# Kernel tuning notes

Measured on AMD Instinct MI355X. Metric: run time of the kernel, lower is better.

## Reference

```python
import jax, jax.numpy as jnp
import numpy as np

N_HEAD = 16
N_EMBD = 2048
B, S = 2, 2048


def setup_inputs() -> dict:
    key = jax.random.key(0)
    k1, k2, k3 = jax.random.split(key, 3)
    scale = 0.02
    return {
        "hidden_states": jax.random.normal(k1, (B, S, N_EMBD), dtype=jnp.float32),
        "attention_mask": jnp.ones((B, S), dtype=jnp.float32),
        "w_attn": jax.random.normal(k2, (N_EMBD, 3 * N_EMBD), dtype=jnp.float32) * scale,
        "b_attn": jnp.zeros((3 * N_EMBD,), dtype=jnp.float32),
        "w_proj": jax.random.normal(k3, (N_EMBD, N_EMBD), dtype=jnp.float32) * scale,
        "b_proj": jnp.zeros((N_EMBD,), dtype=jnp.float32),
    }


def reference(hidden_states, attention_mask, w_attn, b_attn, w_proj, b_proj):
    b, s, d = hidden_states.shape
    h = N_HEAD
    dh = d // h
    qkv = hidden_states @ w_attn + b_attn          # [b, s, 3d]
    q, k, v = jnp.split(qkv, 3, axis=-1)
    # [b, s, d] -> [b, h, s, dh]
    q = q.reshape(b, s, h, dh).transpose(0, 2, 1, 3)
    k = k.reshape(b, s, h, dh).transpose(0, 2, 1, 3)
    v = v.reshape(b, s, h, dh).transpose(0, 2, 1, 3)
    scores = jnp.einsum("bhqd,bhkd->bhqk", q, k) / jnp.sqrt(jnp.float32(dh))
    # padding mask: [b, s] -> additive bias [b, 1, 1, s]
    bias = (1.0 - attention_mask)[:, None, None, :] * -10000.0
    attn = jax.nn.softmax(scores + bias, axis=-1)   # dropout p=0 (eval)
    out = jnp.einsum("bhqk,bhkd->bhqd", attn, v)    # [b, h, s, dh]
    out = out.transpose(0, 2, 1, 3).reshape(b, s, d)
    return out @ w_proj + b_proj
```

## Files before the change

kernel.cpp:

```cpp
#include <hip/hip_runtime.h>
#include <stdint.h>

#define B_   2
#define S_   2048
#define D_   2048
#define NH_  16
#define DH_  128
#define N3_  6144

typedef unsigned short u16;
typedef __bf16 bf16x8 __attribute__((ext_vector_type(8)));
typedef float  f32x4  __attribute__((ext_vector_type(4)));

#define QSCALE   (0.08838834764831845f * 1.4426950408889634f)
#define BIASF    (-10000.0f * 1.4426950408889634f)

__device__ __forceinline__ u16 f2bf(float f) {
  union { float f; unsigned u; } v; v.f = f;
  unsigned u = v.u;
  return (u16)((u + 0x7FFFu + ((u >> 16) & 1u)) >> 16);
}

__device__ __forceinline__ float fast_exp2(float x) {
  float r;
  asm("v_exp_f32 %0, %1" : "=v"(r) : "v"(x));
  return r;
}

#define GL2LDS(gsrc, ldst)                                                              \
  __builtin_amdgcn_global_load_lds((const __attribute__((address_space(1))) void*)(gsrc), \
      (__attribute__((address_space(3))) void*)(ldst), 16, 0, 0)

__device__ __forceinline__ int swz_id() {
  int id = blockIdx.y * gridDim.x + blockIdx.x;
  int cpx = (gridDim.x * gridDim.y) >> 3;
  return (id & 7) * cpx + (id >> 3);
}

__global__ void cvt_kernel(const float* __restrict__ in, u16* __restrict__ out, int n4) {
  int i = blockIdx.x * blockDim.x + threadIdx.x;
  int stride = gridDim.x * blockDim.x;
  for (; i < n4; i += stride) {
    float4 v = ((const float4*)in)[i];
    ushort4 o;
    o.x = f2bf(v.x); o.y = f2bf(v.y); o.z = f2bf(v.z); o.w = f2bf(v.w);
    ((ushort4*)out)[i] = o;
  }
}

__global__ void transpose_kernel(const float* __restrict__ in, u16* __restrict__ out,
                                 int K, int N) {
  __shared__ float tile[32][33];
  int tx = threadIdx.x, ty = threadIdx.y;
  int nx = blockIdx.x * 32, ky = blockIdx.y * 32;
#pragma unroll
  for (int j = 0; j < 32; j += 8)
    tile[ty + j][tx] = in[(size_t)(ky + ty + j) * N + nx + tx];
  __syncthreads();
#pragma unroll
  for (int j = 0; j < 32; j += 8)
    out[(size_t)(nx + ty + j) * K + ky + tx] = f2bf(tile[tx][ty + j]);
}


__device__ __forceinline__ void read_q(const u16* __restrict__ Ab, const u16* __restrict__ Bb,
                                       int wrB, int wcB, int g, int lr,
                                       bf16x8 (&AF)[4][2], bf16x8 (&BF)[2][2]) {
#pragma unroll
  for (int i = 0; i < 4; ++i) {
    int hr = wrB + i * 16 + lr;
#pragma unroll
    for (int kk = 0; kk < 2; ++kk)
      AF[i][kk] = *reinterpret_cast<const bf16x8*>(Ab + hr * 64 + ((((kk << 2) | g) ^ (hr & 7)) * 8));
  }
#pragma unroll
  for (int j = 0; j < 2; ++j) {
    int hbr = wcB + j * 16 + lr;
#pragma unroll
    for (int kk = 0; kk < 2; ++kk)
      BF[j][kk] = *reinterpret_cast<const bf16x8*>(Bb + hbr * 64 + ((((kk << 2) | g) ^ (hbr & 7)) * 8));
  }
}

template <int MS, int NS>
__device__ __forceinline__ void mfma_q(const bf16x8 (&AF)[4][2], const bf16x8 (&BF)[2][2],
                                       f32x4 (&acc)[8][4]) {
  __builtin_amdgcn_s_setprio(1);
#pragma unroll
  for (int i = 0; i < 4; ++i)
#pragma unroll
    for (int j = 0; j < 2; ++j)
#pragma unroll
      for (int kk = 0; kk < 2; ++kk)
        acc[MS * 4 + i][NS * 2 + j] = __builtin_amdgcn_mfma_f32_16x16x32_bf16(
            AF[i][kk], BF[j][kk], acc[MS * 4 + i][NS * 2 + j], 0, 0, 0);
  __builtin_amdgcn_s_setprio(0);
}

template <int KD>
__device__ __forceinline__ void stage_a(const u16* __restrict__ A, u16* lds,
                                        int c, int h, int Tg, int m0, int t) {
#pragma unroll
  for (int inst = 0; inst < 2; ++inst) {
    int idx = inst * 512 + t, hr = idx >> 3, slot = idx & 7;
    int trow = ((hr >> 6) << 7) + h * 64 + (hr & 63);
    GL2LDS(A + (size_t)(m0 + trow) * KD + Tg * 64 + ((slot ^ (hr & 7)) * 8),
           lds + c * 32768 + h * 8192 + idx * 8);
  }
}

template <int KD>
__device__ __forceinline__ void stage_b(const u16* __restrict__ BT, u16* lds,
                                        int c, int h, int Tg, int n0, int t) {
#pragma unroll
  for (int inst = 0; inst < 2; ++inst) {
    int idx = inst * 512 + t, hr = idx >> 3, slot = idx & 7;
    int n = ((hr >> 5) << 6) + h * 32 + (hr & 31);
    GL2LDS(BT + (size_t)(n0 + n) * KD + Tg * 64 + ((slot ^ (hr & 7)) * 8),
           lds + c * 32768 + 16384 + h * 8192 + idx * 8);
  }
}

#define ABASE(c, h) (lds + (c) * 32768 + (h) * 8192)
#define BBASE(c, h) (lds + (c) * 32768 + 16384 + (h) * 8192)
#define VMCNT(n) asm volatile("s_waitcnt vmcnt(" #n ")" ::: "memory")
#define LGKM0                                            \
  do {                                                   \
    asm volatile("s_waitcnt lgkmcnt(0)" ::: "memory");   \
    __builtin_amdgcn_sched_barrier(0);                   \
  } while (0)
#define BAR __builtin_amdgcn_s_barrier()

template <int KD>
__device__ __forceinline__ void gemm256_core(const u16* __restrict__ A, const u16* __restrict__ BT,
                                             int m0, int n0, u16* lds, f32x4 (&acc)[8][4]) {
  const int NT = KD / 64;
  int t = threadIdx.x, wv = t >> 6, lane = t & 63;
  int g = lane >> 4, lr = lane & 15;
  int wrB = (wv >> 2) * 64, wcB = (wv & 3) * 32;
  bf16x8 af0[4][2], bf0[2][2], af1[4][2], bf1[2][2];

  stage_b<KD>(BT, lds, 0, 0, 0, n0, t);
  stage_a<KD>(A, lds, 0, 0, 0, m0, t);
  stage_a<KD>(A, lds, 0, 1, 0, m0, t);
  stage_b<KD>(BT, lds, 0, 1, 0, n0, t);
  stage_b<KD>(BT, lds, 1, 0, 1, n0, t);
  stage_a<KD>(A, lds, 1, 0, 1, m0, t);
  VMCNT(2);
  stage_a<KD>(A, lds, 1, 1, 1, m0, t);
  stage_b<KD>(BT, lds, 1, 1, 1, n0, t);
  BAR;
  read_q(ABASE(0, 0), BBASE(0, 0), wrB, wcB, g, lr, af0, bf0);
  LGKM0;

  for (int T = 0; T < NT; ++T) {
    int c = T & 1;
    read_q(ABASE(c, 1), BBASE(c, 0), wrB, wcB, g, lr, af1, bf1);
    BAR; LGKM0;
    mfma_q<0, 0>(af0, bf0, acc);
    BAR;
    read_q(ABASE(c, 0), BBASE(c, 1), wrB, wcB, g, lr, af0, bf0);
    if (T + 2 < NT) stage_b<KD>(BT, lds, c, 0, T + 2, n0, t);
    BAR; LGKM0;
    mfma_q<1, 0>(af1, bf1, acc);
    BAR;
    read_q(ABASE(c, 1), BBASE(c, 1), wrB, wcB, g, lr, af1, bf1);
    if (T + 2 < NT) stage_a<KD>(A, lds, c, 0, T + 2, m0, t);
    BAR; LGKM0;
    mfma_q<0, 1>(af0, bf0, acc);
    BAR;
    if (T + 2 < NT) {
      VMCNT(2);
      stage_a<KD>(A, lds, c, 1, T + 2, m0, t);
      stage_b<KD>(BT, lds, c, 1, T + 2, n0, t);
    } else {
      VMCNT(0);
    }
    BAR;
    if (T + 1 < NT) read_q(ABASE(c ^ 1, 0), BBASE(c ^ 1, 0), wrB, wcB, g, lr, af0, bf0);
    LGKM0;
    mfma_q<1, 1>(af1, bf1, acc);
    BAR;
  }
}

__global__ __launch_bounds__(512, 1) void gemm_qkv_kernel(
    const u16* __restrict__ A, const u16* __restrict__ BT, const float* __restrict__ bias,
    u16* __restrict__ Qb, u16* __restrict__ Kb, u16* __restrict__ VTb) {
  __shared__ __attribute__((aligned(16))) u16 lds[65536];
  f32x4 acc[8][4] = {};
  int sw = swz_id();
  int n0 = (sw % gridDim.x) * 256, m0 = (sw / gridDim.x) * 256;
  gemm256_core<2048>(A, BT, m0, n0, lds, acc);
  int t = threadIdx.x, lane = t & 63, wv = t >> 6;
  int g = lane >> 4, lr = lane & 15, wr = wv >> 2, wc = wv & 3;
#pragma unroll
  for (int mi = 0; mi < 8; ++mi) {
    int rowbase = m0 + wr * 128 + mi * 16 + g * 4;
    int b = rowbase >> 11, s = rowbase & 2047;
#pragma unroll
    for (int nj = 0; nj < 4; ++nj) {
      int col = n0 + wc * 64 + nj * 16 + lr;
      float bv = bias[col];
      int sec = col >> 11;
      int within = col & 2047;
      int h = within >> 7, d = within & 127;
      if (sec < 2) {
        float mult = (sec == 0) ? QSCALE : 1.0f;
        u16* dst = (sec == 0 ? Qb : Kb) + ((size_t)(b * NH_ + h) * S_ + s) * DH_ + d;
#pragma unroll
        for (int r = 0; r < 4; ++r) dst[(size_t)r * DH_] = f2bf((acc[mi][nj][r] + bv) * mult);
      } else {
        u16* dst = VTb + ((size_t)(b * NH_ + h) * DH_ + d) * S_ + s;
        ushort4 pk;
        pk.x = f2bf(acc[mi][nj][0] + bv); pk.y = f2bf(acc[mi][nj][1] + bv);
        pk.z = f2bf(acc[mi][nj][2] + bv); pk.w = f2bf(acc[mi][nj][3] + bv);
        *reinterpret_cast<ushort4*>(dst) = pk;
      }
    }
  }
}

__global__ __launch_bounds__(512, 1) void gemm_proj_kernel(
    const u16* __restrict__ A, const u16* __restrict__ BT, const float* __restrict__ bias,
    float* __restrict__ out) {
  __shared__ __attribute__((aligned(16))) u16 lds[65536];
  f32x4 acc[8][4] = {};
  int sw = swz_id();
  int n0 = (sw % gridDim.x) * 256, m0 = (sw / gridDim.x) * 256;
  gemm256_core<2048>(A, BT, m0, n0, lds, acc);
  int t = threadIdx.x, lane = t & 63, wv = t >> 6;
  int g = lane >> 4, lr = lane & 15, wr = wv >> 2, wc = wv & 3;
#pragma unroll
  for (int mi = 0; mi < 8; ++mi) {
    int rowbase = m0 + wr * 128 + mi * 16 + g * 4;
#pragma unroll
    for (int nj = 0; nj < 4; ++nj) {
      int col = n0 + wc * 64 + nj * 16 + lr;
      float bv = bias[col];
      float* dst = out + (size_t)rowbase * D_ + col;
#pragma unroll
      for (int r = 0; r < 4; ++r) dst[(size_t)r * D_] = acc[mi][nj][r] + bv;
    }
  }
}

__global__ __launch_bounds__(256) void attn_kernel(
    const u16* __restrict__ Qb, const u16* __restrict__ Kb, const u16* __restrict__ VTb,
    const float* __restrict__ mask, u16* __restrict__ AO) {
  __shared__ __attribute__((aligned(16))) u16 Ks[2][64 * 128];
  __shared__ __attribute__((aligned(16))) u16 Vs[2][128 * 64];
  __shared__ __attribute__((aligned(16))) u16 Ps[4][16 * 64];
  __shared__ float bias_lds[S_];

  int t = threadIdx.x, w = t >> 6, lane = t & 63;
  int g = lane >> 4, lr = lane & 15;
  int sw = swz_id();
  int qt = sw & 31, bh = sw >> 5;
  int b = bh >> 4;
  const u16* Qh = Qb + (size_t)bh * S_ * DH_;
  const u16* Kh = Kb + (size_t)bh * S_ * DH_;
  const u16* Vh = VTb + (size_t)bh * DH_ * S_;
  int q0 = qt * 64 + w * 16;

  for (int i = t; i < S_; i += 256)
    bias_lds[i] = (1.0f - mask[b * S_ + i]) * BIASF;

  bf16x8 aq[4];
#pragma unroll
  for (int kk = 0; kk < 4; ++kk)
    aq[kk] = *reinterpret_cast<const bf16x8*>(Qh + (size_t)(q0 + lr) * DH_ + kk * 32 + g * 8);

  f32x4 oacc[8] = {};
  float m_r[4], l_r[4];
#pragma unroll
  for (int r = 0; r < 4; ++r) { m_r[r] = -1e30f; l_r[r] = 0.f; }

  __syncthreads();

#define STAGE_KV(buf, s0base)                                                    \
  {                                                                              \
    _Pragma("unroll")                                                            \
    for (int i = 0; i < 4; ++i) {                                                \
      int idx = i * 256 + t;                                                     \
      int row = idx >> 4, slot = idx & 15;                                       \
      GL2LDS(Kh + (size_t)((s0base) + row) * DH_ + ((slot ^ (row & 7)) * 8),     \
             &Ks[buf][idx * 8]);                                                 \
    }                                                                            \
    _Pragma("unroll")                                                            \
    for (int i = 0; i < 4; ++i) {                                                \
      int idx = i * 256 + t;                                                     \
      int row = idx >> 3, slot = idx & 7;                                        \
      GL2LDS(Vh + (size_t)row * S_ + (s0base) + ((slot ^ (row & 7)) * 8),        \
             &Vs[buf][idx * 8]);                                                 \
    }                                                                            \
  }

  STAGE_KV(0, 0);
  const int NT = S_ / 64;
  for (int it = 0; it < NT; ++it) {
    int cur = it & 1;
    if (it + 1 < NT) {
      STAGE_KV(cur ^ 1, (it + 1) * 64);
      asm volatile("s_waitcnt vmcnt(8)" ::: "memory");
    } else {
      asm volatile("s_waitcnt vmcnt(0)" ::: "memory");
    }
    __builtin_amdgcn_s_barrier();
    __builtin_amdgcn_sched_barrier(0);

    f32x4 sacc[4] = {};
#pragma unroll
    for (int kk = 0; kk < 4; ++kk) {
#pragma unroll
      for (int n = 0; n < 4; ++n) {
        int c = lr + 16 * n;
        bf16x8 bk = *reinterpret_cast<const bf16x8*>(
            &Ks[cur][c * 128 + ((((kk << 2) | g) ^ (c & 7)) * 8)]);
        sacc[n] = __builtin_amdgcn_mfma_f32_16x16x32_bf16(aq[kk], bk, sacc[n], 0, 0, 0);
      }
    }

    int s0 = it * 64;
    float sv[4][4], mx[4];
#pragma unroll
    for (int r = 0; r < 4; ++r) {
#pragma unroll
      for (int n = 0; n < 4; ++n) sv[r][n] = sacc[n][r] + bias_lds[s0 + lr + 16 * n];
      float m2 = fmaxf(fmaxf(sv[r][0], sv[r][1]), fmaxf(sv[r][2], sv[r][3]));
#pragma unroll
      for (int off = 1; off < 16; off <<= 1) m2 = fmaxf(m2, __shfl_xor(m2, off));
      mx[r] = m2;
    }
    float gmax = fmaxf(fmaxf(mx[0] - m_r[0], mx[1] - m_r[1]),
                       fmaxf(mx[2] - m_r[2], mx[3] - m_r[3]));
    if (__any(gmax > 8.f)) {
#pragma unroll
      for (int r = 0; r < 4; ++r) {
        float mnew = fmaxf(m_r[r], mx[r]);
        float f = fast_exp2(m_r[r] - mnew);
        m_r[r] = mnew;
        l_r[r] *= f;
#pragma unroll
        for (int no = 0; no < 8; ++no) oacc[no][r] *= f;
      }
    }
#pragma unroll
    for (int r = 0; r < 4; ++r) {
      int prow = g * 4 + r;
#pragma unroll
      for (int n = 0; n < 4; ++n) {
        float p = fast_exp2(sv[r][n] - m_r[r]);
        l_r[r] += p;
        int col = lr + 16 * n;
        Ps[w][prow * 64 + ((((col >> 3) ^ (prow & 7)) << 3) + (col & 7))] = f2bf(p);
      }
    }

#pragma unroll
    for (int kk2 = 0; kk2 < 2; ++kk2) {
      bf16x8 ap = *reinterpret_cast<const bf16x8*>(
          &Ps[w][lr * 64 + ((((kk2 << 2) | g) ^ (lr & 7)) * 8)]);
#pragma unroll
      for (int no = 0; no < 8; ++no) {
        int d = lr + 16 * no;
        bf16x8 bv = *reinterpret_cast<const bf16x8*>(
            &Vs[cur][d * 64 + ((((kk2 << 2) | g) ^ (d & 7)) * 8)]);
        oacc[no] = __builtin_amdgcn_mfma_f32_16x16x32_bf16(ap, bv, oacc[no], 0, 0, 0);
      }
    }
    __builtin_amdgcn_sched_barrier(0);
    __builtin_amdgcn_s_barrier();
  }
#undef STAGE_KV

#pragma unroll
  for (int r = 0; r < 4; ++r) {
    float s = l_r[r];
#pragma unroll
    for (int off = 1; off < 16; off <<= 1) s += __shfl_xor(s, off);
    float inv = 1.0f / s;
    int qrow = q0 + g * 4 + r;
    int h = bh & 15;
    u16* dst = AO + ((size_t)(b * S_ + qrow)) * D_ + h * DH_;
#pragma unroll
    for (int no = 0; no < 8; ++no) dst[lr + 16 * no] = f2bf(oacc[no][r] * inv);
  }
}

extern "C" void kernel_launch(void* const* d_in, const int* in_sizes, int n_in,
                              void* d_out, int out_size, void* d_ws, size_t ws_size,
                              hipStream_t stream) {
  const float* h_in   = (const float*)d_in[0];
  const float* mask   = (const float*)d_in[1];
  const float* w_attn = (const float*)d_in[2];
  const float* b_attn = (const float*)d_in[3];
  const float* w_proj = (const float*)d_in[4];
  const float* b_proj = (const float*)d_in[5];
  float* out = (float*)d_out;

  char* ws = (char*)d_ws;
  u16* Hb  = (u16*)(ws);
  u16* W1T = (u16*)(ws + 16777216);
  u16* W2T = (u16*)(ws + 41943040);
  u16* Qb  = (u16*)(ws + 50331648);
  u16* Kb  = (u16*)(ws + 67108864);
  u16* VTb = (u16*)(ws + 83886080);
  u16* AO  = Hb;

  cvt_kernel<<<2048, 256, 0, stream>>>(h_in, Hb, (B_ * S_ * D_) / 4);
  dim3 tb(32, 8);
  transpose_kernel<<<dim3(N3_ / 32, D_ / 32), tb, 0, stream>>>(w_attn, W1T, D_, N3_);
  transpose_kernel<<<dim3(D_ / 32, D_ / 32), tb, 0, stream>>>(w_proj, W2T, D_, D_);
  gemm_qkv_kernel<<<dim3(N3_ / 256, (B_ * S_) / 256), 512, 0, stream>>>(
      Hb, W1T, b_attn, Qb, Kb, VTb);
  attn_kernel<<<dim3(S_ / 64, B_ * NH_), 256, 0, stream>>>(Qb, Kb, VTb, mask, AO);
  gemm_proj_kernel<<<dim3(D_ / 256, (B_ * S_) / 256), 512, 0, stream>>>(AO, W2T, b_proj, out);
}
```

Baseline: 488.7 us.

## Switch GEMMs to 256x128 tiles with split-K LDS halves for two blocks per CU

Both GEMM kernels change from 256x256 output tiles to 256x128 tiles. Each wave now owns a 64x64 subtile, and each 64-wide K step is split into two 32-wide halves with a new row-paired swizzled LDS layout. LDS per block shrinks from 128KB to 96KB, accumulators halve, and launch bounds allow two blocks per CU, so the aim is more blocks in flight to hide latency and better fill the CUs. In exchange, arithmetic intensity per tile drops and global traffic for A grows. The pipeline also has fewer LDS reads and MFMA phases per K step.

```diff
diff --git a/kernel.cpp b/kernel.cpp
--- a/kernel.cpp
+++ b/kernel.cpp
@@ -63,66 +63,8 @@
 }
 
 
-__device__ __forceinline__ void read_q(const u16* __restrict__ Ab, const u16* __restrict__ Bb,
-                                       int wrB, int wcB, int g, int lr,
-                                       bf16x8 (&AF)[4][2], bf16x8 (&BF)[2][2]) {
-#pragma unroll
-  for (int i = 0; i < 4; ++i) {
-    int hr = wrB + i * 16 + lr;
-#pragma unroll
-    for (int kk = 0; kk < 2; ++kk)
-      AF[i][kk] = *reinterpret_cast<const bf16x8*>(Ab + hr * 64 + ((((kk << 2) | g) ^ (hr & 7)) * 8));
-  }
-#pragma unroll
-  for (int j = 0; j < 2; ++j) {
-    int hbr = wcB + j * 16 + lr;
-#pragma unroll
-    for (int kk = 0; kk < 2; ++kk)
-      BF[j][kk] = *reinterpret_cast<const bf16x8*>(Bb + hbr * 64 + ((((kk << 2) | g) ^ (hbr & 7)) * 8));
-  }
-}
-
-template <int MS, int NS>
-__device__ __forceinline__ void mfma_q(const bf16x8 (&AF)[4][2], const bf16x8 (&BF)[2][2],
-                                       f32x4 (&acc)[8][4]) {
-  __builtin_amdgcn_s_setprio(1);
-#pragma unroll
-  for (int i = 0; i < 4; ++i)
-#pragma unroll
-    for (int j = 0; j < 2; ++j)
-#pragma unroll
-      for (int kk = 0; kk < 2; ++kk)
-        acc[MS * 4 + i][NS * 2 + j] = __builtin_amdgcn_mfma_f32_16x16x32_bf16(
-            AF[i][kk], BF[j][kk], acc[MS * 4 + i][NS * 2 + j], 0, 0, 0);
-  __builtin_amdgcn_s_setprio(0);
-}
-
-template <int KD>
-__device__ __forceinline__ void stage_a(const u16* __restrict__ A, u16* lds,
-                                        int c, int h, int Tg, int m0, int t) {
-#pragma unroll
-  for (int inst = 0; inst < 2; ++inst) {
-    int idx = inst * 512 + t, hr = idx >> 3, slot = idx & 7;
-    int trow = ((hr >> 6) << 7) + h * 64 + (hr & 63);
-    GL2LDS(A + (size_t)(m0 + trow) * KD + Tg * 64 + ((slot ^ (hr & 7)) * 8),
-           lds + c * 32768 + h * 8192 + idx * 8);
-  }
-}
-
-template <int KD>
-__device__ __forceinline__ void stage_b(const u16* __restrict__ BT, u16* lds,
-                                        int c, int h, int Tg, int n0, int t) {
-#pragma unroll
-  for (int inst = 0; inst < 2; ++inst) {
-    int idx = inst * 512 + t, hr = idx >> 3, slot = idx & 7;
-    int n = ((hr >> 5) << 6) + h * 32 + (hr & 31);
-    GL2LDS(BT + (size_t)(n0 + n) * KD + Tg * 64 + ((slot ^ (hr & 7)) * 8),
-           lds + c * 32768 + 16384 + h * 8192 + idx * 8);
-  }
-}
-
-#define ABASE(c, h) (lds + (c) * 32768 + (h) * 8192)
-#define BBASE(c, h) (lds + (c) * 32768 + 16384 + (h) * 8192)
+#define KS_ABASE(c, h) (lds + (c) * 24576 + (h) * 8192)
+#define KS_BBASE(c, h) (lds + (c) * 24576 + 16384 + (h) * 4096)
 #define VMCNT(n) asm volatile("s_waitcnt vmcnt(" #n ")" ::: "memory")
 #define LGKM0                                            \
   do {                                                   \
@@ -131,76 +73,119 @@
   } while (0)
 #define BAR __builtin_amdgcn_s_barrier()
 
+__device__ __forceinline__ void ks_read_set(const u16* __restrict__ Ab,
+                                            const u16* __restrict__ Bb,
+                                            int wrB, int wcB, int lr, int g,
+                                            bf16x8 (&af)[4], bf16x8 (&bf)[4]) {
+#pragma unroll
+  for (int i = 0; i < 4; ++i) {
+    int r = wrB + i * 16 + lr;
+    int pr = r >> 1;
+    int slot = (((r & 1) << 2) | g) ^ (pr & 7);
+    af[i] = *reinterpret_cast<const bf16x8*>(Ab + pr * 64 + slot * 8);
+  }
+#pragma unroll
+  for (int j = 0; j < 4; ++j) {
+    int n = wcB + j * 16 + lr;
+    int pn = n >> 1;
+    int slot = (((n & 1) << 2) | g) ^ (pn & 7);
+    bf[j] = *reinterpret_cast<const bf16x8*>(Bb + pn * 64 + slot * 8);
+  }
+}
+
+__device__ __forceinline__ void ks_mfma(const bf16x8 (&af)[4], const bf16x8 (&bf)[4],
+                                        f32x4 (&acc)[4][4]) {
+  __builtin_amdgcn_s_setprio(1);
+#pragma unroll
+  for (int i = 0; i < 4; ++i)
+#pragma unroll
+    for (int j = 0; j < 4; ++j)
+      acc[i][j] = __builtin_amdgcn_mfma_f32_16x16x32_bf16(af[i], bf[j], acc[i][j], 0, 0, 0);
+  __builtin_amdgcn_s_setprio(0);
+}
+
 template <int KD>
-__device__ __forceinline__ void gemm256_core(const u16* __restrict__ A, const u16* __restrict__ BT,
-                                             int m0, int n0, u16* lds, f32x4 (&acc)[8][4]) {
+__device__ __forceinline__ void ks_stage(const u16* __restrict__ A,
+                                         const u16* __restrict__ BT, u16* lds,
+                                         int c, int h, int Tg, int m0, int n0, int t) {
+#pragma unroll
+  for (int inst = 0; inst < 2; ++inst) {
+    int idx = inst * 512 + t;
+    int pr = idx >> 3, s = idx & 7, v = s ^ (pr & 7);
+    int r = pr * 2 + (v >> 2), g = v & 3;
+    GL2LDS(A + (size_t)(m0 + r) * KD + Tg * 64 + h * 32 + g * 8,
+           KS_ABASE(c, h) + idx * 8);
+  }
+  {
+    int idx = t;
+    int pn = idx >> 3, s = idx & 7, v = s ^ (pn & 7);
+    int n = pn * 2 + (v >> 2), g = v & 3;
+    GL2LDS(BT + (size_t)(n0 + n) * KD + Tg * 64 + h * 32 + g * 8,
+           KS_BBASE(c, h) + idx * 8);
+  }
+}
+
+template <int KD>
+__device__ __forceinline__ void gemm_ks_core(const u16* __restrict__ A,
+                                             const u16* __restrict__ BT,
+                                             int m0, int n0, u16* lds, f32x4 (&acc)[4][4]) {
   const int NT = KD / 64;
   int t = threadIdx.x, wv = t >> 6, lane = t & 63;
   int g = lane >> 4, lr = lane & 15;
-  int wrB = (wv >> 2) * 64, wcB = (wv & 3) * 32;
-  bf16x8 af0[4][2], bf0[2][2], af1[4][2], bf1[2][2];
-
-  stage_b<KD>(BT, lds, 0, 0, 0, n0, t);
-  stage_a<KD>(A, lds, 0, 0, 0, m0, t);
-  stage_a<KD>(A, lds, 0, 1, 0, m0, t);
-  stage_b<KD>(BT, lds, 0, 1, 0, n0, t);
-  stage_b<KD>(BT, lds, 1, 0, 1, n0, t);
-  stage_a<KD>(A, lds, 1, 0, 1, m0, t);
-  VMCNT(2);
-  stage_a<KD>(A, lds, 1, 1, 1, m0, t);
-  stage_b<KD>(BT, lds, 1, 1, 1, n0, t);
+  int wrB = (wv >> 1) * 64, wcB = (wv & 1) * 64;
+  bf16x8 af0[4], bf0[4], af1[4], bf1[4];
+
+  ks_stage<KD>(A, BT, lds, 0, 0, 0, m0, n0, t);
+  ks_stage<KD>(A, BT, lds, 0, 1, 0, m0, n0, t);
+  ks_stage<KD>(A, BT, lds, 1, 0, 1, m0, n0, t);
+  ks_stage<KD>(A, BT, lds, 1, 1, 1, m0, n0, t);
+  VMCNT(6);
   BAR;
-  read_q(ABASE(0, 0), BBASE(0, 0), wrB, wcB, g, lr, af0, bf0);
+  ks_read_set(KS_ABASE(0, 0), KS_BBASE(0, 0), wrB, wcB, lr, g, af0, bf0);
   LGKM0;
+  BAR;
 
   for (int T = 0; T < NT; ++T) {
     int c = T & 1;
-    read_q(ABASE(c, 1), BBASE(c, 0), wrB, wcB, g, lr, af1, bf1);
-    BAR; LGKM0;
-    mfma_q<0, 0>(af0, bf0, acc);
+    ks_read_set(KS_ABASE(c, 1), KS_BBASE(c, 1), wrB, wcB, lr, g, af1, bf1);
+    if (T + 2 < NT) ks_stage<KD>(A, BT, lds, c, 0, T + 2, m0, n0, t);
     BAR;
-    read_q(ABASE(c, 0), BBASE(c, 1), wrB, wcB, g, lr, af0, bf0);
-    if (T + 2 < NT) stage_b<KD>(BT, lds, c, 0, T + 2, n0, t);
-    BAR; LGKM0;
-    mfma_q<1, 0>(af1, bf1, acc);
-    BAR;
-    read_q(ABASE(c, 1), BBASE(c, 1), wrB, wcB, g, lr, af1, bf1);
-    if (T + 2 < NT) stage_a<KD>(A, lds, c, 0, T + 2, m0, t);
-    BAR; LGKM0;
-    mfma_q<0, 1>(af0, bf0, acc);
+    LGKM0;
+    ks_mfma(af0, bf0, acc);
     BAR;
     if (T + 2 < NT) {
-      VMCNT(2);
-      stage_a<KD>(A, lds, c, 1, T + 2, m0, t);
-      stage_b<KD>(BT, lds, c, 1, T + 2, n0, t);
+      VMCNT(3);
+      ks_stage<KD>(A, BT, lds, c, 1, T + 2, m0, n0, t);
     } else {
       VMCNT(0);
     }
     BAR;
-    if (T + 1 < NT) read_q(ABASE(c ^ 1, 0), BBASE(c ^ 1, 0), wrB, wcB, g, lr, af0, bf0);
+    if (T + 1 < NT)
+      ks_read_set(KS_ABASE(c ^ 1, 0), KS_BBASE(c ^ 1, 0), wrB, wcB, lr, g, af0, bf0);
     LGKM0;
-    mfma_q<1, 1>(af1, bf1, acc);
+    ks_mfma(af1, bf1, acc);
     BAR;
   }
 }
 
-__global__ __launch_bounds__(512, 1) void gemm_qkv_kernel(
+__global__ __launch_bounds__(512, 2) void gemm_qkv_kernel(
     const u16* __restrict__ A, const u16* __restrict__ BT, const float* __restrict__ bias,
     u16* __restrict__ Qb, u16* __restrict__ Kb, u16* __restrict__ VTb) {
-  __shared__ __attribute__((aligned(16))) u16 lds[65536];
-  f32x4 acc[8][4] = {};
+  __shared__ __attribute__((aligned(16))) u16 lds[49152];
+  f32x4 acc[4][4] = {};
   int sw = swz_id();
-  int n0 = (sw % gridDim.x) * 256, m0 = (sw / gridDim.x) * 256;
-  gemm256_core<2048>(A, BT, m0, n0, lds, acc);
+  int n0 = (sw % gridDim.x) * 128, m0 = (sw / gridDim.x) * 256;
+  gemm_ks_core<2048>(A, BT, m0, n0, lds, acc);
   int t = threadIdx.x, lane = t & 63, wv = t >> 6;
-  int g = lane >> 4, lr = lane & 15, wr = wv >> 2, wc = wv & 3;
-#pragma unroll
-  for (int mi = 0; mi < 8; ++mi) {
-    int rowbase = m0 + wr * 128 + mi * 16 + g * 4;
+  int g = lane >> 4, lr = lane & 15;
+  int wrB = (wv >> 1) * 64, wcB = (wv & 1) * 64;
+#pragma unroll
+  for (int mi = 0; mi < 4; ++mi) {
+    int rowbase = m0 + wrB + mi * 16 + g * 4;
     int b = rowbase >> 11, s = rowbase & 2047;
 #pragma unroll
     for (int nj = 0; nj < 4; ++nj) {
-      int col = n0 + wc * 64 + nj * 16 + lr;
+      int col = n0 + wcB + nj * 16 + lr;
       float bv = bias[col];
       int sec = col >> 11;
       int within = col & 2047;
@@ -221,22 +206,23 @@
   }
 }
 
-__global__ __launch_bounds__(512, 1) void gemm_proj_kernel(
+__global__ __launch_bounds__(512, 2) void gemm_proj_kernel(
     const u16* __restrict__ A, const u16* __restrict__ BT, const float* __restrict__ bias,
     float* __restrict__ out) {
-  __shared__ __attribute__((aligned(16))) u16 lds[65536];
-  f32x4 acc[8][4] = {};
+  __shared__ __attribute__((aligned(16))) u16 lds[49152];
+  f32x4 acc[4][4] = {};
   int sw = swz_id();
-  int n0 = (sw % gridDim.x) * 256, m0 = (sw / gridDim.x) * 256;
-  gemm256_core<2048>(A, BT, m0, n0, lds, acc);
+  int n0 = (sw % gridDim.x) * 128, m0 = (sw / gridDim.x) * 256;
+  gemm_ks_core<2048>(A, BT, m0, n0, lds, acc);
   int t = threadIdx.x, lane = t & 63, wv = t >> 6;
-  int g = lane >> 4, lr = lane & 15, wr = wv >> 2, wc = wv & 3;
-#pragma unroll
-  for (int mi = 0; mi < 8; ++mi) {
-    int rowbase = m0 + wr * 128 + mi * 16 + g * 4;
+  int g = lane >> 4, lr = lane & 15;
+  int wrB = (wv >> 1) * 64, wcB = (wv & 1) * 64;
+#pragma unroll
+  for (int mi = 0; mi < 4; ++mi) {
+    int rowbase = m0 + wrB + mi * 16 + g * 4;
 #pragma unroll
     for (int nj = 0; nj < 4; ++nj) {
-      int col = n0 + wc * 64 + nj * 16 + lr;
+      int col = n0 + wcB + nj * 16 + lr;
       float bv = bias[col];
       float* dst = out + (size_t)rowbase * D_ + col;
 #pragma unroll
@@ -412,8 +398,8 @@
   dim3 tb(32, 8);
   transpose_kernel<<<dim3(N3_ / 32, D_ / 32), tb, 0, stream>>>(w_attn, W1T, D_, N3_);
   transpose_kernel<<<dim3(D_ / 32, D_ / 32), tb, 0, stream>>>(w_proj, W2T, D_, D_);
-  gemm_qkv_kernel<<<dim3(N3_ / 256, (B_ * S_) / 256), 512, 0, stream>>>(
+  gemm_qkv_kernel<<<dim3(N3_ / 128, (B_ * S_) / 256), 512, 0, stream>>>(
       Hb, W1T, b_attn, Qb, Kb, VTb);
   attn_kernel<<<dim3(S_ / 64, B_ * NH_), 256, 0, stream>>>(Qb, Kb, VTb, mask, AO);
-  gemm_proj_kernel<<<dim3(D_ / 256, (B_ * S_) / 256), 512, 0, stream>>>(AO, W2T, b_proj, out);
-}
+  gemm_proj_kernel<<<dim3(D_ / 128, (B_ * S_) / 256), 512, 0, stream>>>(AO, W2T, b_proj, out);
+}
```

Result: faster. 445.3 us (-8.9%).
